# Optimization experiments

Measured on AMD Instinct MI355X. Metric: run time of the kernel, lower is better.

## Reference

```python
import jax, jax.numpy as jnp
import numpy as np

K = 7            # attention window
HEADS = 8
C_ATT = 32       # in_channels of AttBlock
DKH = C_ATT // HEADS  # 4
C_FC = 512       # resnet18 fc channels
NUM_CLASS = 20


def conv2d(x, w, b, stride=1, padding=0):
    out = jax.lax.conv_general_dilated(
        x, w, (stride, stride), [(padding, padding), (padding, padding)],
        dimension_numbers=("NCHW", "OIHW", "NCHW"))
    return out + b[None, :, None, None]


def unfold2(t, k, H, W):
    # torch t.unfold(2,k,1).unfold(3,k,1): [B,C,Hp,Wp] -> [B,C,H,W,k,k]
    t = jnp.stack([t[:, :, i:i + H, :] for i in range(k)], axis=-1)      # [B,C,H,Wp,k]
    t = jnp.stack([t[:, :, :, j:j + W, :] for j in range(k)], axis=-1)   # [B,C,H,W,k,k]
    return t


def bilinear_resize(x, oh, ow):
    # torch F.interpolate(mode='bilinear', align_corners=False)
    B, C, H, W = x.shape
    ys = jnp.clip((jnp.arange(oh, dtype=x.dtype) + 0.5) * (H / oh) - 0.5, 0, H - 1)
    xs = jnp.clip((jnp.arange(ow, dtype=x.dtype) + 0.5) * (W / ow) - 0.5, 0, W - 1)
    y0 = jnp.floor(ys).astype(jnp.int32); y1 = jnp.minimum(y0 + 1, H - 1)
    x0 = jnp.floor(xs).astype(jnp.int32); x1 = jnp.minimum(x0 + 1, W - 1)
    wy = (ys - y0)[None, None, :, None]
    wx = (xs - x0)[None, None, None, :]
    g = lambda yi, xi: x[:, :, yi][:, :, :, xi]
    top = g(y0, x0) * (1 - wx) + g(y0, x1) * wx
    bot = g(y1, x0) * (1 - wx) + g(y1, x1) * wx
    return top * (1 - wy) + bot * wy


def att_block(x, conv1_w, conv1_b, k_w, k_b, q_w, q_b, v_w, v_b, rel_h, rel_w):
    B, _, H, W = x.shape
    x1 = conv2d(x, conv1_w, conv1_b, padding=1)                    # [B,32,H,W]
    p = (K - 1) // 2
    xp = jnp.pad(x1, ((0, 0), (0, 0), (p, K - 1 - p), (p, K - 1 - p)))
    k = conv2d(xp, k_w, k_b)                                       # [B,32,H+6,W+6]
    q = conv2d(x1, q_w, q_b)                                       # [B,32,H,W]
    v = conv2d(xp, v_w, v_b)
    k = unfold2(k, K, H, W).reshape(B, HEADS, H, W, DKH, -1)       # raw row-major reshape (as torch)
    v = unfold2(v, K, H, W).reshape(B, HEADS, H, W, DKH, -1)
    q = q.reshape(B, HEADS, H, W, DKH, 1)
    qk = jnp.matmul(jnp.swapaxes(q, 4, 5), k).reshape(B, HEADS, H, W, K, K)
    # einsum 'bhxydz,cij->bhxyij' fully contracts d,z,c -> outer product of sums
    qsum = q.sum(axis=(4, 5))                                      # [B,heads,H,W]
    rel = rel_h.sum(0) + rel_w.sum(0)                              # [K,1]+[1,K] -> [K,K]
    qk = qk + qsum[..., None, None] * rel
    w = jax.nn.softmax(qk.reshape(B, HEADS, H, W, 1, K * K), axis=-1)
    attn = jnp.matmul(w, jnp.swapaxes(v, 4, 5))                    # [B,heads,H,W,1,dvh]
    return attn.reshape(B, -1, H, W)                               # [B,32,H,W]


def setup_inputs() -> dict:
    key = jax.random.key(0)
    ks = jax.random.split(key, 16)
    s = 0.05
    inp = {
        "x": jax.random.normal(ks[0], (1, 6, 256, 256), jnp.float32),
        "diff_input": 1,
        "backbone_w": jax.random.normal(ks[1], (C_FC, 6, 3, 3), jnp.float32) * s,
        "backbone_b": jax.random.normal(ks[2], (C_FC,), jnp.float32) * s,
        "conv1_w": jax.random.normal(ks[3], (C_ATT, 6, 3, 3), jnp.float32) * s,
        "conv1_b": jax.random.normal(ks[4], (C_ATT,), jnp.float32) * s,
        "k_w": jax.random.normal(ks[5], (C_ATT, C_ATT, 1, 1), jnp.float32) * s,
        "k_b": jax.random.normal(ks[6], (C_ATT,), jnp.float32) * s,
        "q_w": jax.random.normal(ks[7], (C_ATT, C_ATT, 1, 1), jnp.float32) * s,
        "q_b": jax.random.normal(ks[8], (C_ATT,), jnp.float32) * s,
        "v_w": jax.random.normal(ks[9], (C_ATT, C_ATT, 1, 1), jnp.float32) * s,
        "v_b": jax.random.normal(ks[10], (C_ATT,), jnp.float32) * s,
        "rel_h": jax.random.normal(ks[11], (C_ATT // 2, K, 1), jnp.float32),
        "rel_w": jax.random.normal(ks[12], (C_ATT // 2, 1, K), jnp.float32),
        "expand_w": jax.random.normal(ks[13], (C_FC, C_ATT, 3, 3), jnp.float32) * s,
        "expand_b": jax.random.normal(ks[14], (C_FC,), jnp.float32) * s,
        "fc_w": jax.random.normal(ks[15], (NUM_CLASS, C_FC), jnp.float32) * s,
        "fc_b": jnp.zeros((NUM_CLASS,), jnp.float32),
    }
    return inp


def reference(x, diff_input, backbone_w, backbone_b, conv1_w, conv1_b,
              k_w, k_b, q_w, q_b, v_w, v_b, rel_h, rel_w,
              expand_w, expand_b, fc_w, fc_b):
    # multi_task_model stub: stride-8 conv trunk -> [B,512,H/8,W/8]
    res_out = conv2d(x, backbone_w, backbone_b, stride=8, padding=1)
    # diff_input is not None -> attention branch always taken
    att_res = att_block(x, conv1_w, conv1_b, k_w, k_b, q_w, q_b, v_w, v_b, rel_h, rel_w)
    att_scale = bilinear_resize(att_res, res_out.shape[2], res_out.shape[3])
    att_enhance = res_out + conv2d(att_scale, expand_w, expand_b, padding=1)
    pooled = att_enhance.mean(axis=(2, 3))          # AdaptiveAvgPool2d((1,1))
    fc_x = pooled @ fc_w.T + fc_b                   # [B,num_class]
    return fc_x
```

## Files before the change

### kernel.cpp

```cpp
#include <hip/hip_runtime.h>
#include <math.h>


#define OFF_STATA ((size_t)0)
#define OFF_SX    ((size_t)3072)
#define OFF_MG    ((size_t)3136)
#define OFF_MB    ((size_t)8512)
#define OFF_RW    ((size_t)8768)
#define OFF_G     ((size_t)8800)
#define OFF_GB    ((size_t)14560)
#define OFF_FCB2  ((size_t)15640)

#define SM_KT   0
#define SM_VT   2176
#define SM_QS   4352
#define SM_ML   4864
#define SM_BIAS 5032
#define SM_RW   5040
#define SM_RED  5056
#define SM_TOT  5120

__global__ __launch_bounds__(256) void k_prep(
    const float* __restrict__ x,
    const float* __restrict__ c1w, const float* __restrict__ c1b,
    const float* __restrict__ kw, const float* __restrict__ kb,
    const float* __restrict__ qw, const float* __restrict__ qb,
    const float* __restrict__ vw, const float* __restrict__ vb,
    const float* __restrict__ relh, const float* __restrict__ relw,
    const float* __restrict__ bw, const float* __restrict__ bb,
    const float* __restrict__ ew, const float* __restrict__ eb,
    const float* __restrict__ fcw, const float* __restrict__ fcb,
    float* __restrict__ MG, float* __restrict__ MB,
    float* __restrict__ RW, float* __restrict__ Sx,
    float* __restrict__ G, float* __restrict__ Gb,
    float* __restrict__ FCB2) {
  int b = blockIdx.x, t = threadIdx.x;
  __shared__ float red2[256];

  if (b < 32) {
    int c = b;
    if (t < 168) {
      int ci = t / 28, s = t - ci * 28;
      float a = 0.f;
      if (s < 27) {
        int kind = s / 9, t9 = s - kind * 9;
        const float* w3 = (kind == 0 ? kw : (kind == 1 ? vw : qw)) + c * 32;
        #pragma unroll
        for (int m = 0; m < 32; ++m)
          a = fmaf(w3[m], c1w[(m * 6 + ci) * 9 + t9], a);
      }
      MG[c * 168 + t] = a;
    } else if (t < 176) {
      int s = t - 168;
      float a = 0.f;
      if (s < 3) {
        const float* w3 = (s == 0 ? kw : (s == 1 ? vw : qw)) + c * 32;
        a = (s == 0 ? kb : (s == 1 ? vb : qb))[c];
        #pragma unroll
        for (int m = 0; m < 32; ++m) a = fmaf(w3[m], c1b[m], a);
      } else if (s == 3) a = kb[c];
      else if (s == 4) a = vb[c];
      MB[c * 8 + s] = a;
    }
    return;
  }
  if (b < 86) {
    int e = b - 32;
    int ci = e / 9, rem = e - ci * 9, ky = rem / 3, kx = rem - ky * 3;
    const float* xc = x + (size_t)ci * 65536;
    float acc = 0.f;
    for (int p = t; p < 1024; p += 256) {
      int oy = p >> 5, ox = p & 31;
      int ry = 8 * oy - 1 + ky, cx = 8 * ox - 1 + kx;
      if (ry >= 0 && ry <= 255 && cx >= 0 && cx <= 255)
        acc += xc[ry * 256 + cx];
    }
    #pragma unroll
    for (int off = 32; off >= 1; off >>= 1) acc += __shfl_down(acc, off);
    if ((t & 63) == 0) red2[t >> 6] = acc;
    __syncthreads();
    if (t == 0) Sx[e] = red2[0] + red2[1] + red2[2] + red2[3];
    return;
  }
  if (b == 86) {
    if (t < 16) {
      float s = 0.f;
      if (t < 7) {
        for (int cc = 0; cc < 16; ++cc) s += relh[cc * 7 + t];
      } else if (t >= 8 && t < 15) {
        int j = t - 8;
        for (int cc = 0; cc < 16; ++cc) s += relw[cc * 7 + j];
      }
      RW[t] = s;
    }
    return;
  }
  if (b < 194) {
    int gi0 = (b - 87) * 64;
    int l = t & 63, w = t >> 6;
    int g = gi0 + l;
    int o = g / 342;
    int i = g - o * 342;
    bool valid = (g < 6840);
    int oc = valid ? o : 0;
    float acc = 0.f;
    const float* fr = fcw + oc * 512;
    #pragma unroll 8
    for (int mm = 0; mm < 128; ++mm) {
      int m = w * 128 + mm;
      float val = (i < 288) ? ew[m * 288 + i] : bw[m * 54 + (i - 288)];
      acc = fmaf(fr[m], val, acc);
    }
    red2[t] = acc;
    __syncthreads();
    if (w == 0 && valid) {
      float s = red2[l] + red2[64 + l] + red2[128 + l] + red2[192 + l];
      if (i < 288) G[o * 288 + i] = s;
      else         Gb[o * 54 + (i - 288)] = s;
    }
    return;
  }
  {
    int o = b - 194;
    float acc = fmaf(fcw[o * 512 + t], bb[t] + eb[t],
                     fcw[o * 512 + 256 + t] * (bb[256 + t] + eb[256 + t]));
    #pragma unroll
    for (int off = 32; off >= 1; off >>= 1) acc += __shfl_down(acc, off);
    if ((t & 63) == 0) red2[t >> 6] = acc;
    __syncthreads();
    if (t == 0) FCB2[o] = fcb[o] + red2[0] + red2[1] + red2[2] + red2[3];
  }
}

__global__ __launch_bounds__(256) void k_fused(
    const float* __restrict__ x,
    const float* __restrict__ MG, const float* __restrict__ MB,
    const float* __restrict__ RW, float* __restrict__ statA) {
  __shared__ float smem[SM_TOT];
  int tid = threadIdx.x;
  int c  = blockIdx.x >> 5;
  int oy = blockIdx.x & 31;

  float* KT  = smem + SM_KT;
  float* VT  = smem + SM_VT;
  float* QS  = smem + SM_QS;
  float* Ml  = smem + SM_ML;
  float* bsl = smem + SM_BIAS;
  float* rhs = smem + SM_RW;
  float* rws = smem + SM_RW + 8;
  float* red = smem + SM_RED;

  if (tid < 168)      Ml[tid] = MG[c * 168 + tid];
  else if (tid < 176) bsl[tid - 168] = MB[c * 8 + (tid - 168)];
  else if (tid < 192) smem[SM_RW + (tid - 176)] = RW[tid - 176];
  __syncthreads();

  int cg = tid & 63, rg = tid >> 6;
  int roq = (rg == 1) ? 1 : ((rg == 2) ? 0 : -1);
  float kacc[2][4], vacc[2][4], qacc[4];
  {
    float mk = bsl[0], mv = bsl[1], mq = bsl[2];
    #pragma unroll
    for (int ro = 0; ro < 2; ++ro)
      #pragma unroll
      for (int cc = 0; cc < 4; ++cc) { kacc[ro][cc] = mk; vacc[ro][cc] = mv; }
    #pragma unroll
    for (int cc = 0; cc < 4; ++cc) qacc[cc] = mq;
  }
  float mA = (cg > 0) ? 1.0f : 0.0f;
  float mC = (cg < 63) ? 1.0f : 0.0f;
  int xr0 = 8 * oy + 2 * rg - 1;

  #pragma unroll 1
  for (int ci = 0; ci < 6; ++ci) {
    const float* xch = x + (size_t)ci * 65536;
    float wch[28];
    {
      const float4* Mc = (const float4*)&Ml[ci * 28];
      *(float4*)&wch[0]  = Mc[0]; *(float4*)&wch[4]  = Mc[1];
      *(float4*)&wch[8]  = Mc[2]; *(float4*)&wch[12] = Mc[3];
      *(float4*)&wch[16] = Mc[4]; *(float4*)&wch[20] = Mc[5];
      *(float4*)&wch[24] = Mc[6];
    }
    #pragma unroll
    for (int s4 = 0; s4 < 4; ++s4) {
      int xr = xr0 + s4;
      float mrow = (xr >= 0 && xr <= 255) ? 1.0f : 0.0f;
      int xrc = min(max(xr, 0), 255);
      float4 Bv = *(const float4*)&xch[xrc * 256 + 4 * cg];
      float left  = __shfl_up(Bv.w, 1);
      float right = __shfl_down(Bv.x, 1);
      float win[6];
      win[0] = left  * (mA * mrow);
      win[1] = Bv.x * mrow;
      win[2] = Bv.y * mrow;
      win[3] = Bv.z * mrow;
      win[4] = Bv.w * mrow;
      win[5] = right * (mC * mrow);
      if (s4 < 3) {
        const float* wk = &wch[3 * s4];
        const float* wv = &wch[9 + 3 * s4];
        #pragma unroll
        for (int cc = 0; cc < 4; ++cc) {
          float a = kacc[0][cc], b2 = vacc[0][cc];
          #pragma unroll
          for (int dxw = 0; dxw < 3; ++dxw) {
            float xv = win[cc + dxw];
            a  = fmaf(wk[dxw], xv, a);
            b2 = fmaf(wv[dxw], xv, b2);
          }
          kacc[0][cc] = a; vacc[0][cc] = b2;
        }
        if (roq == 0) {
          const float* wq = &wch[18 + 3 * s4];
          #pragma unroll
          for (int cc = 0; cc < 4; ++cc) {
            float qa = qacc[cc];
            #pragma unroll
            for (int dxw = 0; dxw < 3; ++dxw)
              qa = fmaf(wq[dxw], win[cc + dxw], qa);
            qacc[cc] = qa;
          }
        }
      }
      if (s4 >= 1) {
        const float* wk = &wch[3 * (s4 - 1)];
        const float* wv = &wch[9 + 3 * (s4 - 1)];
        #pragma unroll
        for (int cc = 0; cc < 4; ++cc) {
          float a = kacc[1][cc], b2 = vacc[1][cc];
          #pragma unroll
          for (int dxw = 0; dxw < 3; ++dxw) {
            float xv = win[cc + dxw];
            a  = fmaf(wk[dxw], xv, a);
            b2 = fmaf(wv[dxw], xv, b2);
          }
          kacc[1][cc] = a; vacc[1][cc] = b2;
        }
        if (roq == 1) {
          const float* wq = &wch[18 + 3 * (s4 - 1)];
          #pragma unroll
          for (int cc = 0; cc < 4; ++cc) {
            float qa = qacc[cc];
            #pragma unroll
            for (int dxw = 0; dxw < 3; ++dxw)
              qa = fmaf(wq[dxw], win[cc + dxw], qa);
            qacc[cc] = qa;
          }
        }
      }
    }
  }

  #pragma unroll
  for (int ro = 0; ro < 2; ++ro) {
    int r = 2 * rg + ro;
    *(float4*)&KT[r * 272 + 4 * cg + 4] =
        make_float4(kacc[ro][0], kacc[ro][1], kacc[ro][2], kacc[ro][3]);
    *(float4*)&VT[r * 272 + 4 * cg + 4] =
        make_float4(vacc[ro][0], vacc[ro][1], vacc[ro][2], vacc[ro][3]);
  }
  if (roq >= 0)
    *(float4*)&QS[(rg == 2 ? 256 : 0) + 4 * cg] =
        make_float4(qacc[0], qacc[1], qacc[2], qacc[3]);
  if (tid < 96) {
    int t2 = tid;
    int kv = t2 >= 48; if (kv) t2 -= 48;
    int lr = t2 & 7, pi = t2 >> 3;
    int slot = (pi < 3) ? (pi + 1) : (pi + 257);
    (kv ? VT : KT)[lr * 272 + slot] = bsl[3 + kv];
  }
  __syncthreads();

  {
    int half = tid & 1;
    int pix  = tid >> 1;
    int dx   = pix & 1;
    int ox   = (pix >> 1) & 31;
    int dy   = (pix >> 6) & 1;
    int wb   = 8 * ox + 4 * dx;
    int dv   = dx ? 0 : 3;
    int i0   = half * 3;

    float4 qv4 = *(const float4*)&QS[dy * 256 + wb];
    float qv0 = qv4.x, qv1 = qv4.y, qv2 = qv4.z, qv3 = qv4.w;
    float qsum = qv0 + qv1 + qv2 + qv3;

    float sum = 0.f, o = 0.f;
    #pragma unroll
    for (int ii = 0; ii < 4; ++ii) {
      int i = i0 + ii;
      float act = ((half == 0) || (ii > 0)) ? 1.0f : 0.0f;
      const float* kr = &KT[(dy + i) * 272 + wb];
      const float* vr = &VT[(dy + i) * 272 + wb];
      float B[12], BV[12];
      *(float4*)&B[0]  = *(const float4*)&kr[0];
      *(float4*)&B[4]  = *(const float4*)&kr[4];
      *(float4*)&B[8]  = *(const float4*)&kr[8];
      *(float4*)&BV[0] = *(const float4*)&vr[0];
      *(float4*)&BV[4] = *(const float4*)&vr[4];
      *(float4*)&BV[8] = *(const float4*)&vr[8];
      float rh = rhs[i];
      #pragma unroll
      for (int j = 0; j < 7; ++j) {
        float d0 = fmaf(qv0, B[j + 1],
                   fmaf(qv1, B[j + 2],
                   fmaf(qv2, B[j + 3], qv3 * B[j + 4])));
        float s = fmaf(qsum, rh + rws[j], d0);
        float e = act * __expf(s);
        sum += e;
        o = fmaf(e, BV[dv + j + 1], o);
      }
    }
    sum += __shfl_xor(sum, 1);
    o   += __shfl_xor(o, 1);

    float quarter = 0.25f * o / sum;
    float psum = quarter + __shfl_xor(quarter, 2);
    if ((tid & 3) == 0) red[dy * 32 + ox] = psum;
  }
  __syncthreads();

  if (tid < 32) {
    float scv = red[tid] + red[32 + tid];
    float e0  = __shfl(scv, 0, 32);
    float e31 = __shfl(scv, 31, 32);
    float rs = scv;
    #pragma unroll
    for (int off = 16; off >= 1; off >>= 1) rs += __shfl_down(rs, off, 32);
    if (tid == 0) {
      float* pa = statA + (c * 32 + oy) * 3;
      pa[0] = rs; pa[1] = e0; pa[2] = e31;
    }
  }
}

__global__ __launch_bounds__(64) void k_out(
    const float* __restrict__ statA, const float* __restrict__ Sx,
    const float* __restrict__ G, const float* __restrict__ Gb,
    const float* __restrict__ FCB2, float* __restrict__ out) {
  __shared__ float Sl[288];
  __shared__ float SxL[54];
  int o = blockIdx.x, lane = threadIdx.x;
  if (lane < 32) {
    int ch = lane;
    const float* pa = statA + ch * 96;
    float T = 0.f, C0 = 0.f, C31 = 0.f;
    #pragma unroll
    for (int i = 0; i < 32; ++i) {
      T += pa[3 * i]; C0 += pa[3 * i + 1]; C31 += pa[3 * i + 2];
    }
    float r0 = pa[0],  e00 = pa[1],    e0_31 = pa[2];
    float r31 = pa[93], e31_0 = pa[94], e31_31 = pa[95];
    #pragma unroll
    for (int ky = 0; ky < 3; ++ky) {
      float exR = (ky == 0) ? r31 : (ky == 2 ? r0 : 0.f);
      #pragma unroll
      for (int kx = 0; kx < 3; ++kx) {
        float exC = (kx == 0) ? C31 : (kx == 2 ? C0 : 0.f);
        float corner = 0.f;
        if (ky != 1 && kx != 1) {
          if (ky == 0) corner = (kx == 0) ? e31_31 : e31_0;
          else         corner = (kx == 0) ? e0_31  : e00;
        }
        Sl[ch * 9 + ky * 3 + kx] = T - exR - exC + corner;
      }
    }
  } else {
    for (int idx = lane - 32; idx < 54; idx += 32) SxL[idx] = Sx[idx];
  }
  __syncthreads();

  float acc = 0.f;
  #pragma unroll
  for (int i0 = 0; i0 < 288; i0 += 64) {
    int i = i0 + lane;
    if (i < 288) acc = fmaf(G[o * 288 + i], Sl[i], acc);
  }
  if (lane < 54) acc = fmaf(Gb[o * 54 + lane], SxL[lane], acc);
  #pragma unroll
  for (int off = 32; off >= 1; off >>= 1) acc += __shfl_down(acc, off);
  if (lane == 0) out[o] = FCB2[o] + acc * (1.0f / 1024.0f);
}

extern "C" void kernel_launch(void* const* d_in, const int* in_sizes, int n_in,
                              void* d_out, int out_size, void* d_ws, size_t ws_size,
                              hipStream_t stream) {
  const float* x    = (const float*)d_in[0];
  const float* bw   = (const float*)d_in[2];
  const float* bb   = (const float*)d_in[3];
  const float* c1w  = (const float*)d_in[4];
  const float* c1b  = (const float*)d_in[5];
  const float* kw   = (const float*)d_in[6];
  const float* kb   = (const float*)d_in[7];
  const float* qw   = (const float*)d_in[8];
  const float* qb   = (const float*)d_in[9];
  const float* vw   = (const float*)d_in[10];
  const float* vb   = (const float*)d_in[11];
  const float* relh = (const float*)d_in[12];
  const float* relw = (const float*)d_in[13];
  const float* ew   = (const float*)d_in[14];
  const float* eb   = (const float*)d_in[15];
  const float* fcw  = (const float*)d_in[16];
  const float* fcb  = (const float*)d_in[17];

  float* ws    = (float*)d_ws;
  float* statA = ws + OFF_STATA;
  float* Sxb   = ws + OFF_SX;
  float* MG    = ws + OFF_MG;
  float* MB    = ws + OFF_MB;
  float* RW    = ws + OFF_RW;
  float* Gm    = ws + OFF_G;
  float* Gbm   = ws + OFF_GB;
  float* FCB2  = ws + OFF_FCB2;
  float* out   = (float*)d_out;

  k_prep <<<214,  256, 0, stream>>>(x, c1w, c1b, kw, kb, qw, qb, vw, vb,
                                    relh, relw, bw, bb, ew, eb, fcw, fcb,
                                    MG, MB, RW, Sxb, Gm, Gbm, FCB2);
  k_fused<<<1024, 256, 0, stream>>>(x, MG, MB, RW, statA);
  k_out  <<<20,   64,  0, stream>>>(statA, Sxb, Gm, Gbm, FCB2, out);
}
```

Measured before the change: 35.60 us.

## Merge prep kernel into fused kernel and compute folded weights per block

Removes the separate k_prep launch. Each attention block now recomputes its channel's folded conv1·k/v/q weights and rel sums directly in shared memory, and the independent prep tasks (Sx sums, G/Gb folding, FCB2) run as extra blocks appended to the same grid. Out-of-range input rows are now skipped with a continue instead of being clamped and masked. This saves one kernel launch and the global round trip for the folded weights, at the cost of redundant weight folding in every block (32 blocks per channel) and a somewhat longer startup per block.

```diff
diff --git a/kernel.cpp b/kernel.cpp
--- a/kernel.cpp
+++ b/kernel.cpp
@@ -4,12 +4,9 @@
 
 #define OFF_STATA ((size_t)0)
 #define OFF_SX    ((size_t)3072)
-#define OFF_MG    ((size_t)3136)
-#define OFF_MB    ((size_t)8512)
-#define OFF_RW    ((size_t)8768)
-#define OFF_G     ((size_t)8800)
-#define OFF_GB    ((size_t)14560)
-#define OFF_FCB2  ((size_t)15640)
+#define OFF_G     ((size_t)3136)
+#define OFF_GB    ((size_t)8896)
+#define OFF_FCB2  ((size_t)9976)
 
 #define SM_KT   0
 #define SM_VT   2176
@@ -20,7 +17,7 @@
 #define SM_RED  5056
 #define SM_TOT  5120
 
-__global__ __launch_bounds__(256) void k_prep(
+__global__ __launch_bounds__(256) void k_fused(
     const float* __restrict__ x,
     const float* __restrict__ c1w, const float* __restrict__ c1b,
     const float* __restrict__ kw, const float* __restrict__ kb,
@@ -30,116 +27,73 @@
     const float* __restrict__ bw, const float* __restrict__ bb,
     const float* __restrict__ ew, const float* __restrict__ eb,
     const float* __restrict__ fcw, const float* __restrict__ fcb,
-    float* __restrict__ MG, float* __restrict__ MB,
-    float* __restrict__ RW, float* __restrict__ Sx,
+    float* __restrict__ statA, float* __restrict__ Sx,
     float* __restrict__ G, float* __restrict__ Gb,
     float* __restrict__ FCB2) {
-  int b = blockIdx.x, t = threadIdx.x;
-  __shared__ float red2[256];
-
-  if (b < 32) {
-    int c = b;
-    if (t < 168) {
-      int ci = t / 28, s = t - ci * 28;
-      float a = 0.f;
-      if (s < 27) {
-        int kind = s / 9, t9 = s - kind * 9;
-        const float* w3 = (kind == 0 ? kw : (kind == 1 ? vw : qw)) + c * 32;
-        #pragma unroll
-        for (int m = 0; m < 32; ++m)
-          a = fmaf(w3[m], c1w[(m * 6 + ci) * 9 + t9], a);
-      }
-      MG[c * 168 + t] = a;
-    } else if (t < 176) {
-      int s = t - 168;
-      float a = 0.f;
-      if (s < 3) {
-        const float* w3 = (s == 0 ? kw : (s == 1 ? vw : qw)) + c * 32;
-        a = (s == 0 ? kb : (s == 1 ? vb : qb))[c];
-        #pragma unroll
-        for (int m = 0; m < 32; ++m) a = fmaf(w3[m], c1b[m], a);
-      } else if (s == 3) a = kb[c];
-      else if (s == 4) a = vb[c];
-      MB[c * 8 + s] = a;
-    }
-    return;
-  }
-  if (b < 86) {
-    int e = b - 32;
-    int ci = e / 9, rem = e - ci * 9, ky = rem / 3, kx = rem - ky * 3;
-    const float* xc = x + (size_t)ci * 65536;
-    float acc = 0.f;
-    for (int p = t; p < 1024; p += 256) {
-      int oy = p >> 5, ox = p & 31;
-      int ry = 8 * oy - 1 + ky, cx = 8 * ox - 1 + kx;
-      if (ry >= 0 && ry <= 255 && cx >= 0 && cx <= 255)
-        acc += xc[ry * 256 + cx];
-    }
-    #pragma unroll
-    for (int off = 32; off >= 1; off >>= 1) acc += __shfl_down(acc, off);
-    if ((t & 63) == 0) red2[t >> 6] = acc;
-    __syncthreads();
-    if (t == 0) Sx[e] = red2[0] + red2[1] + red2[2] + red2[3];
-    return;
-  }
-  if (b == 86) {
-    if (t < 16) {
-      float s = 0.f;
-      if (t < 7) {
-        for (int cc = 0; cc < 16; ++cc) s += relh[cc * 7 + t];
-      } else if (t >= 8 && t < 15) {
-        int j = t - 8;
-        for (int cc = 0; cc < 16; ++cc) s += relw[cc * 7 + j];
-      }
-      RW[t] = s;
-    }
-    return;
-  }
-  if (b < 194) {
-    int gi0 = (b - 87) * 64;
-    int l = t & 63, w = t >> 6;
-    int g = gi0 + l;
-    int o = g / 342;
-    int i = g - o * 342;
-    bool valid = (g < 6840);
-    int oc = valid ? o : 0;
-    float acc = 0.f;
-    const float* fr = fcw + oc * 512;
-    #pragma unroll 8
-    for (int mm = 0; mm < 128; ++mm) {
-      int m = w * 128 + mm;
-      float val = (i < 288) ? ew[m * 288 + i] : bw[m * 54 + (i - 288)];
-      acc = fmaf(fr[m], val, acc);
-    }
-    red2[t] = acc;
-    __syncthreads();
-    if (w == 0 && valid) {
-      float s = red2[l] + red2[64 + l] + red2[128 + l] + red2[192 + l];
-      if (i < 288) G[o * 288 + i] = s;
-      else         Gb[o * 54 + (i - 288)] = s;
-    }
-    return;
-  }
-  {
-    int o = b - 194;
-    float acc = fmaf(fcw[o * 512 + t], bb[t] + eb[t],
-                     fcw[o * 512 + 256 + t] * (bb[256 + t] + eb[256 + t]));
-    #pragma unroll
-    for (int off = 32; off >= 1; off >>= 1) acc += __shfl_down(acc, off);
-    if ((t & 63) == 0) red2[t >> 6] = acc;
-    __syncthreads();
-    if (t == 0) FCB2[o] = fcb[o] + red2[0] + red2[1] + red2[2] + red2[3];
-  }
-}
-
-__global__ __launch_bounds__(256) void k_fused(
-    const float* __restrict__ x,
-    const float* __restrict__ MG, const float* __restrict__ MB,
-    const float* __restrict__ RW, float* __restrict__ statA) {
   __shared__ float smem[SM_TOT];
   int tid = threadIdx.x;
-  int c  = blockIdx.x >> 5;
-  int oy = blockIdx.x & 31;
+  int bid = blockIdx.x;
+
+  if (bid >= 1024) {
+    float* red2 = smem;
+    if (bid < 1078) {
+      int e = bid - 1024;
+      int ci = e / 9, rem = e - ci * 9, ky = rem / 3, kx = rem - ky * 3;
+      const float* xc = x + (size_t)ci * 65536;
+      float acc = 0.f;
+      for (int p = tid; p < 1024; p += 256) {
+        int oy = p >> 5, ox = p & 31;
+        int ry = 8 * oy - 1 + ky, cx = 8 * ox - 1 + kx;
+        if (ry >= 0 && ry <= 255 && cx >= 0 && cx <= 255)
+          acc += xc[ry * 256 + cx];
+      }
+      #pragma unroll
+      for (int off = 32; off >= 1; off >>= 1) acc += __shfl_down(acc, off);
+      if ((tid & 63) == 0) red2[tid >> 6] = acc;
+      __syncthreads();
+      if (tid == 0) Sx[e] = red2[0] + red2[1] + red2[2] + red2[3];
+      return;
+    }
+    if (bid < 1185) {
+      int gi0 = (bid - 1078) * 64;
+      int l = tid & 63, w = tid >> 6;
+      int g = gi0 + l;
+      int o = g / 342;
+      int i = g - o * 342;
+      bool valid = (g < 6840);
+      int oc = valid ? o : 0;
+      float acc = 0.f;
+      const float* fr = fcw + oc * 512;
+      #pragma unroll 8
+      for (int mm = 0; mm < 128; ++mm) {
+        int m = w * 128 + mm;
+        float val = (i < 288) ? ew[m * 288 + i] : bw[m * 54 + (i - 288)];
+        acc = fmaf(fr[m], val, acc);
+      }
+      red2[tid] = acc;
+      __syncthreads();
+      if (w == 0 && valid) {
+        float s = red2[l] + red2[64 + l] + red2[128 + l] + red2[192 + l];
+        if (i < 288) G[o * 288 + i] = s;
+        else         Gb[o * 54 + (i - 288)] = s;
+      }
+      return;
+    }
+    {
+      int o = bid - 1185;
+      float acc = fmaf(fcw[o * 512 + tid], bb[tid] + eb[tid],
+                       fcw[o * 512 + 256 + tid] * (bb[256 + tid] + eb[256 + tid]));
+      #pragma unroll
+      for (int off = 32; off >= 1; off >>= 1) acc += __shfl_down(acc, off);
+      if ((tid & 63) == 0) red2[tid >> 6] = acc;
+      __syncthreads();
+      if (tid == 0) FCB2[o] = fcb[o] + red2[0] + red2[1] + red2[2] + red2[3];
+      return;
+    }
+  }
+
+  int c  = bid >> 5;
+  int oy = bid & 31;
 
   float* KT  = smem + SM_KT;
   float* VT  = smem + SM_VT;
@@ -150,9 +104,42 @@
   float* rws = smem + SM_RW + 8;
   float* red = smem + SM_RED;
 
-  if (tid < 168)      Ml[tid] = MG[c * 168 + tid];
-  else if (tid < 176) bsl[tid - 168] = MB[c * 8 + (tid - 168)];
-  else if (tid < 192) smem[SM_RW + (tid - 176)] = RW[tid - 176];
+  if (tid < 168) {
+    int ci = tid / 28, s = tid - ci * 28;
+    if (s < 27) {
+      int kind = s / 9, t9 = s - kind * 9;
+      const float* w3 = (kind == 0 ? kw : (kind == 1 ? vw : qw)) + c * 32;
+      float a = 0.f;
+      #pragma unroll
+      for (int m = 0; m < 32; ++m)
+        a = fmaf(w3[m], c1w[(m * 6 + ci) * 9 + t9], a);
+      Ml[ci * 28 + s] = a;
+    }
+  } else if (tid < 176) {
+    int s = tid - 168;
+    if (s < 3) {
+      const float* w3 = (s == 0 ? kw : (s == 1 ? vw : qw)) + c * 32;
+      float a = (s == 0 ? kb : (s == 1 ? vb : qb))[c];
+      #pragma unroll
+      for (int m = 0; m < 32; ++m) a = fmaf(w3[m], c1b[m], a);
+      bsl[s] = a;
+    } else if (s == 3) bsl[3] = kb[c];
+    else if (s == 4) bsl[4] = vb[c];
+  } else if (tid < 184) {
+    int i = tid - 176;
+    if (i < 7) {
+      float s = 0.f;
+      for (int cc = 0; cc < 16; ++cc) s += relh[cc * 7 + i];
+      rhs[i] = s;
+    }
+  } else if (tid < 192) {
+    int j = tid - 184;
+    if (j < 7) {
+      float s = 0.f;
+      for (int cc = 0; cc < 16; ++cc) s += relw[cc * 7 + j];
+      rws[j] = s;
+    }
+  }
   __syncthreads();
 
   int cg = tid & 63, rg = tid >> 6;
@@ -185,18 +172,17 @@
     #pragma unroll
     for (int s4 = 0; s4 < 4; ++s4) {
       int xr = xr0 + s4;
-      float mrow = (xr >= 0 && xr <= 255) ? 1.0f : 0.0f;
-      int xrc = min(max(xr, 0), 255);
-      float4 Bv = *(const float4*)&xch[xrc * 256 + 4 * cg];
+      if (xr < 0 || xr > 255) continue;
+      float4 Bv = *(const float4*)&xch[xr * 256 + 4 * cg];
       float left  = __shfl_up(Bv.w, 1);
       float right = __shfl_down(Bv.x, 1);
       float win[6];
-      win[0] = left  * (mA * mrow);
-      win[1] = Bv.x * mrow;
-      win[2] = Bv.y * mrow;
-      win[3] = Bv.z * mrow;
-      win[4] = Bv.w * mrow;
-      win[5] = right * (mC * mrow);
+      win[0] = left * mA;
+      win[1] = Bv.x;
+      win[2] = Bv.y;
+      win[3] = Bv.z;
+      win[4] = Bv.w;
+      win[5] = right * mC;
       if (s4 < 3) {
         const float* wk = &wch[3 * s4];
         const float* wv = &wch[9 + 3 * s4];
@@ -407,17 +393,13 @@
   float* ws    = (float*)d_ws;
   float* statA = ws + OFF_STATA;
   float* Sxb   = ws + OFF_SX;
-  float* MG    = ws + OFF_MG;
-  float* MB    = ws + OFF_MB;
-  float* RW    = ws + OFF_RW;
   float* Gm    = ws + OFF_G;
   float* Gbm   = ws + OFF_GB;
   float* FCB2  = ws + OFF_FCB2;
   float* out   = (float*)d_out;
 
-  k_prep <<<214,  256, 0, stream>>>(x, c1w, c1b, kw, kb, qw, qb, vw, vb,
+  k_fused<<<1205, 256, 0, stream>>>(x, c1w, c1b, kw, kb, qw, qb, vw, vb,
                                     relh, relw, bw, bb, ew, eb, fcw, fcb,
-                                    MG, MB, RW, Sxb, Gm, Gbm, FCB2);
-  k_fused<<<1024, 256, 0, stream>>>(x, MG, MB, RW, statA);
+                                    statA, Sxb, Gm, Gbm, FCB2);
   k_out  <<<20,   64,  0, stream>>>(statA, Sxb, Gm, Gbm, FCB2, out);
 }
```

Result: faster. 29.79 us (-16.3%).
